# Kernel tuning notes

Hardware: AMD Instinct MI355X
Metric: run time of the kernel (lower is better)

## Reference

```python
import jax, jax.numpy as jnp
import numpy as np

NUM_HEADS = 8
HEAD_DIM = 64  # hidden_dim // num_heads = 512 // 8
THRESHOLD = 0.5


def setup_inputs() -> dict:
    key = jax.random.key(0)
    ks = jax.random.split(key, 12)
    B, T, D, Hd = 4, 1024, 512, 512
    s = 0.02
    inp = {
        'x': jax.random.normal(ks[0], (B, T, D), dtype=jnp.float32),
        'Wq': jax.random.normal(ks[1], (D, Hd), dtype=jnp.float32) * s,
        'bq': jnp.zeros((Hd,), jnp.float32),
        'Wk': jax.random.normal(ks[2], (D, Hd), dtype=jnp.float32) * s,
        'bk': jnp.zeros((Hd,), jnp.float32),
        'Wv': jax.random.normal(ks[3], (D, Hd), dtype=jnp.float32) * s,
        'bv': jnp.zeros((Hd,), jnp.float32),
        'conv_w': jax.random.normal(ks[4], (NUM_HEADS,), dtype=jnp.float32) * 0.3,
        'conv_b': jnp.zeros((1,), jnp.float32),
        'Wfh': jax.random.normal(ks[5], (Hd, Hd), dtype=jnp.float32) * s,
        'bfh': jnp.zeros((Hd,), jnp.float32),
        'Wfg': jax.random.normal(ks[6], (Hd, Hd), dtype=jnp.float32) * s,
        'bfg': jnp.zeros((Hd,), jnp.float32),
        'Wrh': jax.random.normal(ks[7], (Hd, Hd), dtype=jnp.float32) * s,
        'brh': jnp.zeros((Hd,), jnp.float32),
        'Wrg': jax.random.normal(ks[8], (Hd, Hd), dtype=jnp.float32) * s,
        'brg': jnp.zeros((Hd,), jnp.float32),
    }
    return inp


def reference(x, Wq, bq, Wk, bk, Wv, bv, conv_w, conv_b,
              Wfh, bfh, Wfg, bfg, Wrh, brh, Wrg, brg):
    B, T, D = x.shape
    H, hd = NUM_HEADS, HEAD_DIM
    scale = hd ** -0.5

    q = (x @ Wq + bq).reshape(B, T, H, hd).transpose(0, 2, 1, 3)  # [B,H,T,hd]
    k = (x @ Wk + bk).reshape(B, T, H, hd).transpose(0, 2, 1, 3)
    v = (x @ Wv + bv).reshape(B, T, H, hd).transpose(0, 2, 1, 3)

    scores = jnp.einsum('bhqd,bhkd->bhqk', q, k) * scale        # [B,H,T,T]
    A_t = jax.nn.softmax(scores, axis=-1)

    # cross-head 1x1 conv: weighted sum over heads -> [B,1,T,T]
    R_f = jax.nn.sigmoid(jnp.einsum('bhqk,h->bqk', A_t, conv_w) + conv_b[0])
    R_f = R_f[:, None]                                           # [B,1,T,T]
    M_f = (R_f <= THRESHOLD).astype(A_t.dtype)
    M_r = (1.0 - R_f <= THRESHOLD).astype(A_t.dtype)

    A_f = jax.nn.softmax(A_t * M_f, axis=-1)
    A_r = jax.nn.softmax(A_t * M_r, axis=-1)

    T_f = jnp.einsum('bhqk,bhkd->bhqd', A_f, v).transpose(0, 2, 1, 3).reshape(B, T, H * hd)
    T_r = jnp.einsum('bhqk,bhkd->bhqd', A_r, v).transpose(0, 2, 1, 3).reshape(B, T, H * hd)

    F_f = T_f @ Wfh + bfh
    G_f = jax.nn.sigmoid(T_f @ Wfg + bfg)
    F_r = T_r @ Wrh + brh
    G_r = jax.nn.sigmoid(T_r @ Wrg + brg)

    G_cat = jax.nn.softmax(jnp.stack([G_f, G_r], axis=-1), axis=-1)  # [B,T,Hd,2]
    F_t = F_f * G_cat[..., 0] + F_r * G_cat[..., 1]
    return F_t
```

## Files before the change

kernel.cpp:

```cpp
#include <hip/hip_runtime.h>
#include <hip/hip_bf16.h>
#include <stdint.h>

typedef short bf16x8 __attribute__((ext_vector_type(8)));
typedef float f32x4 __attribute__((ext_vector_type(4)));

__device__ __forceinline__ unsigned short f2bf(float f) {
  union { float f; unsigned int u; } v;
  v.f = f;
  unsigned int u = v.u;
  u = (u + 0x7fffu + ((u >> 16) & 1u)) >> 16;
  return (unsigned short)u;
}

__device__ __forceinline__ unsigned int cvt_pk_bf16(float lo, float hi) {
  unsigned int r;
  asm("v_cvt_pk_bf16_f32 %0, %1, %2" : "=v"(r) : "v"(lo), "v"(hi));
  return r;
}

typedef union { bf16x8 v; unsigned int u[4]; } frag_u;

__device__ __forceinline__ void gload16(const void* g, void* lds) {
  __builtin_amdgcn_global_load_lds(
      (const __attribute__((address_space(1))) unsigned int*)(unsigned long long)g,
      (__attribute__((address_space(3))) unsigned int*)(unsigned long long)(unsigned)(unsigned long long)lds,
      16, 0, 0);
}

__device__ __forceinline__ bf16x8 lds_frag(const unsigned short* t, int row, int ch4q) {
  return *(const bf16x8*)(t + row * 64 + ((ch4q ^ (row & 7)) << 3));
}


__global__ __launch_bounds__(256) void prep_kernel(
    const float* __restrict__ x,
    const float* __restrict__ Wq, const float* __restrict__ Wk, const float* __restrict__ Wv,
    const float* __restrict__ Wfh, const float* __restrict__ Wfg,
    const float* __restrict__ Wrh, const float* __restrict__ Wrg,
    unsigned short* __restrict__ xb, unsigned short* __restrict__ wt) {
  int bid = blockIdx.x;
  int tid = threadIdx.x;
  if (bid < 256) {
    const float4* xi = (const float4*)x;
#pragma unroll
    for (int rep = 0; rep < 8; rep++) {
      int i = bid * 256 + tid + rep * 65536;
      float4 v = xi[i];
      uint2 u;
      u.x = cvt_pk_bf16(v.x, v.y);
      u.y = cvt_pk_bf16(v.z, v.w);
      *(uint2*)&xb[(size_t)i * 4] = u;
    }
  } else {
    __shared__ float tile[64][65];
    int t = bid - 256;
    int mat = t >> 6;
    t &= 63;
    int tr = (t >> 3) * 64, tc = (t & 7) * 64;
    const float* W = (mat == 0) ? Wq : (mat == 1) ? Wk : (mat == 2) ? Wv
                   : (mat == 3) ? Wfh : (mat == 4) ? Wfg : (mat == 5) ? Wrh : Wrg;
    unsigned short* Wt = wt + (size_t)mat * 512 * 512;
    for (int rep = 0; rep < 16; rep++) {
      int idx = rep * 256 + tid;
      int r = idx >> 6, c = idx & 63;
      tile[r][c] = W[(tr + r) * 512 + tc + c];
    }
    __syncthreads();
    for (int rep = 0; rep < 16; rep++) {
      int idx = rep * 256 + tid;
      int r = idx >> 6, c = idx & 63;
      Wt[(tc + r) * 512 + tr + c] = f2bf(tile[c][r]);
    }
  }
}

__global__ __launch_bounds__(256, 2) void qkv_kernel(
    const unsigned short* __restrict__ xb,
    const unsigned short* __restrict__ wtq, const unsigned short* __restrict__ wtk,
    const unsigned short* __restrict__ wtv,
    const float* __restrict__ bq, const float* __restrict__ bk, const float* __restrict__ bv,
    unsigned short* __restrict__ Qfrag, unsigned short* __restrict__ Kfrag,
    unsigned short* __restrict__ Vfrag) {
  __shared__ __attribute__((aligned(16))) unsigned short smem[32768];
  unsigned short* st0 = smem;
  unsigned short* st1 = smem + 4608;
  unsigned short* st2 = smem + 9216;
  const int m0 = blockIdx.y * 64, n0 = blockIdx.x * 64;
  const int tid = threadIdx.x, w = tid >> 6, lane = tid & 63;
  const int c = lane & 15, quad = lane >> 4;
  const int wm = w & 1, wn = w >> 1;
  const int rsel = lane >> 3, csel = lane & 7;
  const int sc = csel ^ rsel;
  const char* Ag  = (const char*)xb  + (size_t)(m0 + w * 16 + rsel) * 1024 + sc * 16;
  const char* Bgq = (const char*)wtq + (size_t)(n0 + w * 16 + rsel) * 1024 + sc * 16;
  const char* Bgk = (const char*)wtk + (size_t)(n0 + w * 16 + rsel) * 1024 + sc * 16;
  const char* Bgv = (const char*)wtv + (size_t)(n0 + w * 16 + rsel) * 1024 + sc * 16;
  const int woff = w * 1024;

  f32x4 acc[3][2][2];
  f32x4 z4 = {0.f, 0.f, 0.f, 0.f};
#pragma unroll
  for (int o = 0; o < 3; o++)
#pragma unroll
    for (int i = 0; i < 2; i++)
#pragma unroll
      for (int j = 0; j < 2; j++) acc[o][i][j] = z4;

  {
    unsigned short* base = smem;
    gload16(Ag, base + woff);              gload16(Ag + 8192, base + woff + 512);
    gload16(Bgq, base + 4096 + woff);      gload16(Bgq + 8192, base + 4096 + woff + 512);
    gload16(Bgk, base + 8192 + woff);      gload16(Bgk + 8192, base + 8192 + woff + 512);
    gload16(Bgv, base + 12288 + woff);     gload16(Bgv + 8192, base + 12288 + woff + 512);
  }
  __syncthreads();

  for (int ks = 0; ks < 8; ks++) {
    unsigned short* cur = smem + (ks & 1) * 16384;
    if (ks < 7) {
      unsigned short* nxt = smem + ((ks + 1) & 1) * 16384;
      const int kb = (ks + 1) * 128;
      gload16(Ag + kb, nxt + woff);          gload16(Ag + kb + 8192, nxt + woff + 512);
      gload16(Bgq + kb, nxt + 4096 + woff);  gload16(Bgq + kb + 8192, nxt + 4096 + woff + 512);
      gload16(Bgk + kb, nxt + 8192 + woff);  gload16(Bgk + kb + 8192, nxt + 8192 + woff + 512);
      gload16(Bgv + kb, nxt + 12288 + woff); gload16(Bgv + kb + 8192, nxt + 12288 + woff + 512);
    }
#pragma unroll
    for (int ch = 0; ch < 2; ch++) {
      const int cq = ch * 4 + quad;
      bf16x8 a0 = lds_frag(cur, wm * 32 + c, cq);
      bf16x8 a1 = lds_frag(cur, wm * 32 + 16 + c, cq);
#pragma unroll
      for (int nt = 0; nt < 2; nt++) {
        const int rb = wn * 32 + nt * 16 + c;
        bf16x8 fq = lds_frag(cur + 4096, rb, cq);
        bf16x8 fk = lds_frag(cur + 8192, rb, cq);
        bf16x8 fv = lds_frag(cur + 12288, rb, cq);
        acc[0][0][nt] = __builtin_amdgcn_mfma_f32_16x16x32_bf16(a0, fq, acc[0][0][nt], 0, 0, 0);
        acc[0][1][nt] = __builtin_amdgcn_mfma_f32_16x16x32_bf16(a1, fq, acc[0][1][nt], 0, 0, 0);
        acc[1][0][nt] = __builtin_amdgcn_mfma_f32_16x16x32_bf16(a0, fk, acc[1][0][nt], 0, 0, 0);
        acc[1][1][nt] = __builtin_amdgcn_mfma_f32_16x16x32_bf16(a1, fk, acc[1][1][nt], 0, 0, 0);
        acc[2][0][nt] = __builtin_amdgcn_mfma_f32_16x16x32_bf16(a0, fv, acc[2][0][nt], 0, 0, 0);
        acc[2][1][nt] = __builtin_amdgcn_mfma_f32_16x16x32_bf16(a1, fv, acc[2][1][nt], 0, 0, 0);
      }
    }
    __syncthreads();
  }

#pragma unroll
  for (int ms = 0; ms < 2; ms++)
#pragma unroll
    for (int nt = 0; nt < 2; nt++) {
      int n_l = wn * 32 + nt * 16 + c;
      int n = n0 + n_l;
      float biasq = bq[n], biask = bk[n], biasv = bv[n];
#pragma unroll
      for (int r = 0; r < 4; r++) {
        int m_l = wm * 32 + ms * 16 + quad * 4 + r;
        st0[m_l * 72 + n_l] = f2bf((acc[0][ms][nt][r] + biasq) * 0.125f);
        st1[m_l * 72 + n_l] = f2bf(acc[1][ms][nt][r] + biask);
        st2[n_l * 72 + m_l] = f2bf(acc[2][ms][nt][r] + biasv);
      }
    }
  __syncthreads();

  {
    const int h = n0 >> 6;
    const int bb = m0 >> 10, t0b = (m0 & 1023) >> 4;
#pragma unroll
    for (int sub = 0; sub < 2; sub++) {
      uint4 vq = *(uint4*)&st0[(w * 16 + c) * 72 + sub * 32 + quad * 8];
      uint4 vk = *(uint4*)&st1[(w * 16 + c) * 72 + sub * 32 + quad * 8];
      size_t base = (size_t)((bb * 64 + t0b + w) * 8192) + h * 1024 + sub * 512 + lane * 8;
      *(uint4*)&Qfrag[base] = vq;
      *(uint4*)&Kfrag[base] = vk;
    }
    const int ktq = t0b + w;
    const int ktp = ktq >> 1, half = ktq & 1;
#pragma unroll
    for (int dm = 0; dm < 4; dm++) {
      uint2 vv = *(uint2*)&st2[(dm * 16 + c) * 72 + w * 16 + quad * 4];
      size_t base = (size_t)(bb * 8 + h) * 65536 + (size_t)(ktp * 4 + dm) * 512
                  + lane * 8 + half * 4;
      *(uint2*)&Vfrag[base] = vv;
    }
  }
}

__global__ __launch_bounds__(512, 2) void attn_kernel(
    const unsigned short* __restrict__ Qfrag, const unsigned short* __restrict__ Kfrag,
    const unsigned short* __restrict__ Vfrag,
    const float* __restrict__ conv_w, const float* __restrict__ conv_b,
    unsigned short* __restrict__ Tfb, unsigned short* __restrict__ Trb) {
  const int b = blockIdx.x, qt = blockIdx.y;
  const int tid = threadIdx.x, w = tid >> 6, lane = tid & 63;
  const int c = lane & 15, quad = lane >> 4;
  __shared__ float zbuf[8][16];
  __shared__ float izbuf[8][16];
  __shared__ __attribute__((aligned(16))) float red[2 * 8 * 4 * 64 * 4];
  __shared__ float zred[2][8][16];

  f32x4 z4 = {0.f, 0.f, 0.f, 0.f};
  const float cb = conv_b[0];
  const size_t qbase = (size_t)((b * 64 + qt) * 8192) + lane * 8;
  const size_t kb0 = (size_t)((b * 64 + w * 8) * 8192) + lane * 8;
  const size_t vb0 = (size_t)(b * 8) * 65536 + lane * 8;

  f32x4 g[8];
#pragma unroll
  for (int j = 0; j < 8; j++) g[j] = {cb, cb, cb, cb};

  for (int h = 0; h < 8; h++) {
    bf16x8 qf0 = *(const bf16x8*)&Qfrag[qbase + h * 1024];
    bf16x8 qf1 = *(const bf16x8*)&Qfrag[qbase + h * 1024 + 512];
    f32x4 p[8];
    float zh = 0.f;
#pragma unroll
    for (int j = 0; j < 8; j++) {
      const size_t kb = kb0 + (size_t)j * 8192 + h * 1024;
      bf16x8 kf0 = *(const bf16x8*)&Kfrag[kb];
      bf16x8 kf1 = *(const bf16x8*)&Kfrag[kb + 512];
      f32x4 s = __builtin_amdgcn_mfma_f32_16x16x32_bf16(kf0, qf0, z4, 0, 0, 0);
      s = __builtin_amdgcn_mfma_f32_16x16x32_bf16(kf1, qf1, s, 0, 0, 0);
      p[j][0] = __expf(s[0]); p[j][1] = __expf(s[1]);
      p[j][2] = __expf(s[2]); p[j][3] = __expf(s[3]);
      zh += (p[j][0] + p[j][1]) + (p[j][2] + p[j][3]);
    }
    zh += __shfl_xor(zh, 16); zh += __shfl_xor(zh, 32);
    __syncthreads();
    if (quad == 0) zbuf[w][c] = zh;
    __syncthreads();
    float Z = ((zbuf[0][c] + zbuf[1][c]) + (zbuf[2][c] + zbuf[3][c]))
            + ((zbuf[4][c] + zbuf[5][c]) + (zbuf[6][c] + zbuf[7][c]));
    const float izq = 1.0f / Z;
    if (w == 0 && quad == 0) izbuf[h][c] = izq;
    const float cwz = conv_w[h] * izq;
#pragma unroll
    for (int j = 0; j < 8; j++) {
      g[j][0] += cwz * p[j][0]; g[j][1] += cwz * p[j][1];
      g[j][2] += cwz * p[j][2]; g[j][3] += cwz * p[j][3];
    }
  }

  unsigned int mmx[4], mmy[4];
#pragma unroll
  for (int t = 0; t < 4; t++) {
    unsigned int p0 = 0, p1 = 0;
#pragma unroll
    for (int r = 0; r < 4; r++) {
      p0 |= ((g[2 * t][r] <= 0.f ? 1u : 0u) | (g[2 * t][r] >= 0.f ? 2u : 0u)) << (8 * r);
      p1 |= ((g[2 * t + 1][r] <= 0.f ? 1u : 0u) | (g[2 * t + 1][r] >= 0.f ? 2u : 0u)) << (8 * r);
    }
    mmx[t] = p0; mmy[t] = p1;
  }
  __syncthreads();

  frag_u ones;
  ones.u[0] = 0x3F803F80u; ones.u[1] = 0x3F803F80u;
  ones.u[2] = 0x3F803F80u; ones.u[3] = 0x3F803F80u;

  const int fr = w >> 2, dmslot = w & 3;
  const size_t tbase = (size_t)(b * 1024 + qt * 16 + c) * 512;
  unsigned short* dstsel = (fr == 0) ? Tfb : Trb;

  for (int h = 0; h < 8; h++) {
    bf16x8 qf0 = *(const bf16x8*)&Qfrag[qbase + h * 1024];
    bf16x8 qf1 = *(const bf16x8*)&Qfrag[qbase + h * 1024 + 512];
    const float iz_h = izbuf[h][c];
    f32x4 accf[4], accr[4];
#pragma unroll
    for (int i = 0; i < 4; i++) { accf[i] = z4; accr[i] = z4; }
    f32x4 zf4 = z4, zr4 = z4;
#pragma unroll
    for (int t = 0; t < 4; t++) {
      const size_t kba = kb0 + (size_t)(2 * t) * 8192 + h * 1024;
      const size_t kbb = kba + 8192;
      bf16x8 ka0 = *(const bf16x8*)&Kfrag[kba];
      bf16x8 ka1 = *(const bf16x8*)&Kfrag[kba + 512];
      bf16x8 kb0f = *(const bf16x8*)&Kfrag[kbb];
      bf16x8 kb1f = *(const bf16x8*)&Kfrag[kbb + 512];
      f32x4 sa = __builtin_amdgcn_mfma_f32_16x16x32_bf16(ka0, qf0, z4, 0, 0, 0);
      sa = __builtin_amdgcn_mfma_f32_16x16x32_bf16(ka1, qf1, sa, 0, 0, 0);
      f32x4 sb = __builtin_amdgcn_mfma_f32_16x16x32_bf16(kb0f, qf0, z4, 0, 0, 0);
      sb = __builtin_amdgcn_mfma_f32_16x16x32_bf16(kb1f, qf1, sb, 0, 0, 0);
      float ea[4], eb[4];
#pragma unroll
      for (int r = 0; r < 4; r++) {
        ea[r] = __expf(__expf(sa[r]) * iz_h);
        eb[r] = __expf(__expf(sb[r]) * iz_h);
      }
      frag_u pF, pR;
      pF.u[0] = cvt_pk_bf16((mmx[t] & 0x1u)       ? ea[0] : 1.f, (mmx[t] & 0x100u)     ? ea[1] : 1.f);
      pF.u[1] = cvt_pk_bf16((mmx[t] & 0x10000u)   ? ea[2] : 1.f, (mmx[t] & 0x1000000u) ? ea[3] : 1.f);
      pF.u[2] = cvt_pk_bf16((mmy[t] & 0x1u)       ? eb[0] : 1.f, (mmy[t] & 0x100u)     ? eb[1] : 1.f);
      pF.u[3] = cvt_pk_bf16((mmy[t] & 0x10000u)   ? eb[2] : 1.f, (mmy[t] & 0x1000000u) ? eb[3] : 1.f);
      pR.u[0] = cvt_pk_bf16((mmx[t] & 0x2u)       ? ea[0] : 1.f, (mmx[t] & 0x200u)     ? ea[1] : 1.f);
      pR.u[1] = cvt_pk_bf16((mmx[t] & 0x20000u)   ? ea[2] : 1.f, (mmx[t] & 0x2000000u) ? ea[3] : 1.f);
      pR.u[2] = cvt_pk_bf16((mmy[t] & 0x2u)       ? eb[0] : 1.f, (mmy[t] & 0x200u)     ? eb[1] : 1.f);
      pR.u[3] = cvt_pk_bf16((mmy[t] & 0x20000u)   ? eb[2] : 1.f, (mmy[t] & 0x2000000u) ? eb[3] : 1.f);
      zf4 = __builtin_amdgcn_mfma_f32_16x16x32_bf16(ones.v, pF.v, zf4, 0, 0, 0);
      zr4 = __builtin_amdgcn_mfma_f32_16x16x32_bf16(ones.v, pR.v, zr4, 0, 0, 0);
      const size_t vbh = vb0 + (size_t)h * 65536 + (size_t)((w * 4 + t) * 4) * 512;
#pragma unroll
      for (int dm = 0; dm < 4; dm++) {
        bf16x8 vf = *(const bf16x8*)&Vfrag[vbh + (size_t)dm * 512];
        accf[dm] = __builtin_amdgcn_mfma_f32_16x16x32_bf16(vf, pF.v, accf[dm], 0, 0, 0);
        accr[dm] = __builtin_amdgcn_mfma_f32_16x16x32_bf16(vf, pR.v, accr[dm], 0, 0, 0);
      }
    }
    __syncthreads();
#pragma unroll
    for (int dm = 0; dm < 4; dm++) {
      *(f32x4*)&red[(((0 * 8 + w) * 4 + dm) * 64 + lane) * 4] = accf[dm];
      *(f32x4*)&red[(((1 * 8 + w) * 4 + dm) * 64 + lane) * 4] = accr[dm];
    }
    if (quad == 0) { zred[0][w][c] = zf4[0]; zred[1][w][c] = zr4[0]; }
    __syncthreads();
    {
      f32x4 o = z4;
#pragma unroll
      for (int w2 = 0; w2 < 8; w2++)
        o += *(const f32x4*)&red[(((fr * 8 + w2) * 4 + dmslot) * 64 + lane) * 4];
      float Zq = 0.f;
#pragma unroll
      for (int w2 = 0; w2 < 8; w2++) Zq += zred[fr][w2][c];
      const float iz = 1.0f / Zq;
      uint2 u;
      u.x = cvt_pk_bf16(o[0] * iz, o[1] * iz);
      u.y = cvt_pk_bf16(o[2] * iz, o[3] * iz);
      *(uint2*)&dstsel[tbase + h * 64 + dmslot * 16 + quad * 4] = u;
    }
  }
}

__global__ __launch_bounds__(256, 2) void final_kernel(
    const unsigned short* __restrict__ Tfb, const unsigned short* __restrict__ Trb,
    const unsigned short* __restrict__ wfh, const unsigned short* __restrict__ wfg,
    const unsigned short* __restrict__ wrh, const unsigned short* __restrict__ wrg,
    const float* __restrict__ bfh, const float* __restrict__ bfg,
    const float* __restrict__ brh, const float* __restrict__ brg,
    float* __restrict__ out) {
  __shared__ __attribute__((aligned(16))) unsigned short smem[2][20480];
  const int m0 = blockIdx.y * 32, n0 = blockIdx.x * 64;
  const int tid = threadIdx.x, w = tid >> 6, lane = tid & 63;
  const int c = lane & 15, quad = lane >> 4;
  const int wm = w & 1, wn = w >> 1;
  const int rsel = lane >> 3, csel = lane & 7;
  const int sc = csel ^ rsel;
  const char* Agf = (const char*)Tfb + (size_t)(m0 + w * 8 + rsel) * 1024 + sc * 16;
  const char* Agr = (const char*)Trb + (size_t)(m0 + w * 8 + rsel) * 1024 + sc * 16;
  const char* Bg0 = (const char*)wfh + (size_t)(n0 + w * 16 + rsel) * 1024 + sc * 16;
  const char* Bg1 = (const char*)wfg + (size_t)(n0 + w * 16 + rsel) * 1024 + sc * 16;
  const char* Bg2 = (const char*)wrh + (size_t)(n0 + w * 16 + rsel) * 1024 + sc * 16;
  const char* Bg3 = (const char*)wrg + (size_t)(n0 + w * 16 + rsel) * 1024 + sc * 16;
  const int aoff = w * 512;
  const int boff = w * 1024;

  f32x4 acc[4][2];
  f32x4 z4 = {0.f, 0.f, 0.f, 0.f};
#pragma unroll
  for (int o = 0; o < 4; o++)
#pragma unroll
    for (int j = 0; j < 2; j++) acc[o][j] = z4;

  {
    unsigned short* nb = smem[0];
    gload16(Agf, nb + aoff);
    gload16(Agr, nb + 2048 + aoff);
    gload16(Bg0, nb + 4096 + boff);   gload16(Bg0 + 8192, nb + 4096 + boff + 512);
    gload16(Bg1, nb + 8192 + boff);   gload16(Bg1 + 8192, nb + 8192 + boff + 512);
    gload16(Bg2, nb + 12288 + boff);  gload16(Bg2 + 8192, nb + 12288 + boff + 512);
    gload16(Bg3, nb + 16384 + boff);  gload16(Bg3 + 8192, nb + 16384 + boff + 512);
  }
  __syncthreads();

  for (int ks = 0; ks < 8; ks++) {
    unsigned short* cur = smem[ks & 1];
    if (ks < 7) {
      unsigned short* nb = smem[(ks + 1) & 1];
      const int kb = (ks + 1) * 128;
      gload16(Agf + kb, nb + aoff);
      gload16(Agr + kb, nb + 2048 + aoff);
      gload16(Bg0 + kb, nb + 4096 + boff);   gload16(Bg0 + kb + 8192, nb + 4096 + boff + 512);
      gload16(Bg1 + kb, nb + 8192 + boff);   gload16(Bg1 + kb + 8192, nb + 8192 + boff + 512);
      gload16(Bg2 + kb, nb + 12288 + boff);  gload16(Bg2 + kb + 8192, nb + 12288 + boff + 512);
      gload16(Bg3 + kb, nb + 16384 + boff);  gload16(Bg3 + kb + 8192, nb + 16384 + boff + 512);
    }
#pragma unroll
    for (int ch = 0; ch < 2; ch++) {
      const int cq = ch * 4 + quad;
      bf16x8 af = lds_frag(cur, wm * 16 + c, cq);
      bf16x8 ar = lds_frag(cur + 2048, wm * 16 + c, cq);
#pragma unroll
      for (int nt = 0; nt < 2; nt++) {
        const int rb = wn * 32 + nt * 16 + c;
        bf16x8 f0 = lds_frag(cur + 4096, rb, cq);
        bf16x8 f1 = lds_frag(cur + 8192, rb, cq);
        bf16x8 f2 = lds_frag(cur + 12288, rb, cq);
        bf16x8 f3 = lds_frag(cur + 16384, rb, cq);
        acc[0][nt] = __builtin_amdgcn_mfma_f32_16x16x32_bf16(af, f0, acc[0][nt], 0, 0, 0);
        acc[1][nt] = __builtin_amdgcn_mfma_f32_16x16x32_bf16(af, f1, acc[1][nt], 0, 0, 0);
        acc[2][nt] = __builtin_amdgcn_mfma_f32_16x16x32_bf16(ar, f2, acc[2][nt], 0, 0, 0);
        acc[3][nt] = __builtin_amdgcn_mfma_f32_16x16x32_bf16(ar, f3, acc[3][nt], 0, 0, 0);
      }
    }
    __syncthreads();
  }

#pragma unroll
  for (int nt = 0; nt < 2; nt++) {
    int n = n0 + wn * 32 + nt * 16 + c;
    float b0 = bfh[n], b1 = bfg[n], b2 = brh[n], b3 = brg[n];
    int t0 = m0 + wm * 16 + quad * 4;
#pragma unroll
    for (int r = 0; r < 4; r++) {
      int t = t0 + r;
      float Ff = acc[0][nt][r] + b0;
      float Gf = 1.0f / (1.0f + __expf(-(acc[1][nt][r] + b1)));
      float Fr = acc[2][nt][r] + b2;
      float Gr = 1.0f / (1.0f + __expf(-(acc[3][nt][r] + b3)));
      float ef = __expf(Gf), er = __expf(Gr);
      out[(size_t)t * 512 + n] = (Ff * ef + Fr * er) / (ef + er);
    }
  }
}

extern "C" void kernel_launch(void* const* d_in, const int* in_sizes, int n_in,
                              void* d_out, int out_size, void* d_ws, size_t ws_size,
                              hipStream_t stream) {
  const float* x   = (const float*)d_in[0];
  const float* Wq  = (const float*)d_in[1];
  const float* bq  = (const float*)d_in[2];
  const float* Wk  = (const float*)d_in[3];
  const float* bk  = (const float*)d_in[4];
  const float* Wv  = (const float*)d_in[5];
  const float* bv  = (const float*)d_in[6];
  const float* cw  = (const float*)d_in[7];
  const float* cb  = (const float*)d_in[8];
  const float* Wfh = (const float*)d_in[9];
  const float* bfh = (const float*)d_in[10];
  const float* Wfg = (const float*)d_in[11];
  const float* bfg = (const float*)d_in[12];
  const float* Wrh = (const float*)d_in[13];
  const float* brh = (const float*)d_in[14];
  const float* Wrg = (const float*)d_in[15];
  const float* brg = (const float*)d_in[16];

  char* ws = (char*)d_ws;
  const size_t MB = 1024 * 1024;
  unsigned short* xb    = (unsigned short*)(ws + 0 * MB);
  unsigned short* Qfrag = (unsigned short*)(ws + 4 * MB);
  unsigned short* Kfrag = (unsigned short*)(ws + 8 * MB);
  unsigned short* Vfrag = (unsigned short*)(ws + 12 * MB);
  unsigned short* Tfb   = (unsigned short*)(ws + 16 * MB);
  unsigned short* Trb   = (unsigned short*)(ws + 20 * MB);
  unsigned short* wt    = (unsigned short*)(ws + 24 * MB);
  const size_t WSZ = 512 * 512;

  prep_kernel<<<704, 256, 0, stream>>>(x, Wq, Wk, Wv, Wfh, Wfg, Wrh, Wrg, xb, wt);
  qkv_kernel<<<dim3(8, 64), 256, 0, stream>>>(xb, wt + 0 * WSZ, wt + 1 * WSZ, wt + 2 * WSZ,
                                              bq, bk, bv, Qfrag, Kfrag, Vfrag);
  attn_kernel<<<dim3(4, 64), 512, 0, stream>>>(Qfrag, Kfrag, Vfrag, cw, cb, Tfb, Trb);
  final_kernel<<<dim3(8, 128), 256, 0, stream>>>(Tfb, Trb, wt + 3 * WSZ, wt + 4 * WSZ,
                                                 wt + 5 * WSZ, wt + 6 * WSZ,
                                                 bfh, bfg, brh, brg, (float*)d_out);
}
```

Before: 176.7 us.

## Fuse output gating GEMMs into attention kernel via LDS-staged T tiles

The attention kernel now writes its per-block T_f/T_r tiles (16 rows x 512) into shared memory instead of global buffers. Each of its 8 waves then computes a 64-column slice of the four output projections with MFMA and applies the gated softmax combine directly. This removes the separate final_kernel launch and the global round trip of the T buffers. In exchange, every attention block streams all four 512x512 weight matrices straight from global/L2 with no LDS reuse, and shared memory per block grows.

Result: slower. 224.5 us (+27.1%).

```diff
diff --git a/kernel.cpp b/kernel.cpp
--- a/kernel.cpp
+++ b/kernel.cpp
@@ -192,7 +192,11 @@
     const unsigned short* __restrict__ Qfrag, const unsigned short* __restrict__ Kfrag,
     const unsigned short* __restrict__ Vfrag,
     const float* __restrict__ conv_w, const float* __restrict__ conv_b,
-    unsigned short* __restrict__ Tfb, unsigned short* __restrict__ Trb) {
+    const unsigned short* __restrict__ wfh, const unsigned short* __restrict__ wfg,
+    const unsigned short* __restrict__ wrh, const unsigned short* __restrict__ wrg,
+    const float* __restrict__ bfh, const float* __restrict__ bfg,
+    const float* __restrict__ brh, const float* __restrict__ brg,
+    float* __restrict__ out) {
   const int b = blockIdx.x, qt = blockIdx.y;
   const int tid = threadIdx.x, w = tid >> 6, lane = tid & 63;
   const int c = lane & 15, quad = lane >> 4;
@@ -200,6 +204,7 @@
   __shared__ float izbuf[8][16];
   __shared__ __attribute__((aligned(16))) float red[2 * 8 * 4 * 64 * 4];
   __shared__ float zred[2][8][16];
+  __shared__ __attribute__((aligned(16))) unsigned short ts[2][16][520];
 
   f32x4 z4 = {0.f, 0.f, 0.f, 0.f};
   const float cb = conv_b[0];
@@ -261,8 +266,6 @@
   ones.u[2] = 0x3F803F80u; ones.u[3] = 0x3F803F80u;
 
   const int fr = w >> 2, dmslot = w & 3;
-  const size_t tbase = (size_t)(b * 1024 + qt * 16 + c) * 512;
-  unsigned short* dstsel = (fr == 0) ? Tfb : Trb;
 
   for (int h = 0; h < 8; h++) {
     bf16x8 qf0 = *(const bf16x8*)&Qfrag[qbase + h * 1024];
@@ -329,99 +332,52 @@
       uint2 u;
       u.x = cvt_pk_bf16(o[0] * iz, o[1] * iz);
       u.y = cvt_pk_bf16(o[2] * iz, o[3] * iz);
-      *(uint2*)&dstsel[tbase + h * 64 + dmslot * 16 + quad * 4] = u;
-    }
-  }
-}
-
-__global__ __launch_bounds__(256, 2) void final_kernel(
-    const unsigned short* __restrict__ Tfb, const unsigned short* __restrict__ Trb,
-    const unsigned short* __restrict__ wfh, const unsigned short* __restrict__ wfg,
-    const unsigned short* __restrict__ wrh, const unsigned short* __restrict__ wrg,
-    const float* __restrict__ bfh, const float* __restrict__ bfg,
-    const float* __restrict__ brh, const float* __restrict__ brg,
-    float* __restrict__ out) {
-  __shared__ __attribute__((aligned(16))) unsigned short smem[2][20480];
-  const int m0 = blockIdx.y * 32, n0 = blockIdx.x * 64;
-  const int tid = threadIdx.x, w = tid >> 6, lane = tid & 63;
-  const int c = lane & 15, quad = lane >> 4;
-  const int wm = w & 1, wn = w >> 1;
-  const int rsel = lane >> 3, csel = lane & 7;
-  const int sc = csel ^ rsel;
-  const char* Agf = (const char*)Tfb + (size_t)(m0 + w * 8 + rsel) * 1024 + sc * 16;
-  const char* Agr = (const char*)Trb + (size_t)(m0 + w * 8 + rsel) * 1024 + sc * 16;
-  const char* Bg0 = (const char*)wfh + (size_t)(n0 + w * 16 + rsel) * 1024 + sc * 16;
-  const char* Bg1 = (const char*)wfg + (size_t)(n0 + w * 16 + rsel) * 1024 + sc * 16;
-  const char* Bg2 = (const char*)wrh + (size_t)(n0 + w * 16 + rsel) * 1024 + sc * 16;
-  const char* Bg3 = (const char*)wrg + (size_t)(n0 + w * 16 + rsel) * 1024 + sc * 16;
-  const int aoff = w * 512;
-  const int boff = w * 1024;
-
-  f32x4 acc[4][2];
-  f32x4 z4 = {0.f, 0.f, 0.f, 0.f};
-#pragma unroll
-  for (int o = 0; o < 4; o++)
-#pragma unroll
-    for (int j = 0; j < 2; j++) acc[o][j] = z4;
+      *(uint2*)&ts[fr][c][h * 64 + dmslot * 16 + quad * 4] = u;
+    }
+  }
+  __syncthreads();
 
   {
-    unsigned short* nb = smem[0];
-    gload16(Agf, nb + aoff);
-    gload16(Agr, nb + 2048 + aoff);
-    gload16(Bg0, nb + 4096 + boff);   gload16(Bg0 + 8192, nb + 4096 + boff + 512);
-    gload16(Bg1, nb + 8192 + boff);   gload16(Bg1 + 8192, nb + 8192 + boff + 512);
-    gload16(Bg2, nb + 12288 + boff);  gload16(Bg2 + 8192, nb + 12288 + boff + 512);
-    gload16(Bg3, nb + 16384 + boff);  gload16(Bg3 + 8192, nb + 16384 + boff + 512);
-  }
-  __syncthreads();
-
-  for (int ks = 0; ks < 8; ks++) {
-    unsigned short* cur = smem[ks & 1];
-    if (ks < 7) {
-      unsigned short* nb = smem[(ks + 1) & 1];
-      const int kb = (ks + 1) * 128;
-      gload16(Agf + kb, nb + aoff);
-      gload16(Agr + kb, nb + 2048 + aoff);
-      gload16(Bg0 + kb, nb + 4096 + boff);   gload16(Bg0 + kb + 8192, nb + 4096 + boff + 512);
-      gload16(Bg1 + kb, nb + 8192 + boff);   gload16(Bg1 + kb + 8192, nb + 8192 + boff + 512);
-      gload16(Bg2 + kb, nb + 12288 + boff);  gload16(Bg2 + kb + 8192, nb + 12288 + boff + 512);
-      gload16(Bg3 + kb, nb + 16384 + boff);  gload16(Bg3 + kb + 8192, nb + 16384 + boff + 512);
-    }
-#pragma unroll
-    for (int ch = 0; ch < 2; ch++) {
-      const int cq = ch * 4 + quad;
-      bf16x8 af = lds_frag(cur, wm * 16 + c, cq);
-      bf16x8 ar = lds_frag(cur + 2048, wm * 16 + c, cq);
-#pragma unroll
-      for (int nt = 0; nt < 2; nt++) {
-        const int rb = wn * 32 + nt * 16 + c;
-        bf16x8 f0 = lds_frag(cur + 4096, rb, cq);
-        bf16x8 f1 = lds_frag(cur + 8192, rb, cq);
-        bf16x8 f2 = lds_frag(cur + 12288, rb, cq);
-        bf16x8 f3 = lds_frag(cur + 16384, rb, cq);
-        acc[0][nt] = __builtin_amdgcn_mfma_f32_16x16x32_bf16(af, f0, acc[0][nt], 0, 0, 0);
-        acc[1][nt] = __builtin_amdgcn_mfma_f32_16x16x32_bf16(af, f1, acc[1][nt], 0, 0, 0);
-        acc[2][nt] = __builtin_amdgcn_mfma_f32_16x16x32_bf16(ar, f2, acc[2][nt], 0, 0, 0);
-        acc[3][nt] = __builtin_amdgcn_mfma_f32_16x16x32_bf16(ar, f3, acc[3][nt], 0, 0, 0);
-      }
-    }
-    __syncthreads();
-  }
-
-#pragma unroll
-  for (int nt = 0; nt < 2; nt++) {
-    int n = n0 + wn * 32 + nt * 16 + c;
-    float b0 = bfh[n], b1 = bfg[n], b2 = brh[n], b3 = brg[n];
-    int t0 = m0 + wm * 16 + quad * 4;
-#pragma unroll
-    for (int r = 0; r < 4; r++) {
-      int t = t0 + r;
-      float Ff = acc[0][nt][r] + b0;
-      float Gf = 1.0f / (1.0f + __expf(-(acc[1][nt][r] + b1)));
-      float Fr = acc[2][nt][r] + b2;
-      float Gr = 1.0f / (1.0f + __expf(-(acc[3][nt][r] + b3)));
-      float ef = __expf(Gf), er = __expf(Gr);
-      out[(size_t)t * 512 + n] = (Ff * ef + Fr * er) / (ef + er);
+    const int n0w = w * 64;
+    const size_t r0 = (size_t)(b * 1024 + qt * 16);
+    f32x4 oa[4][4];
+#pragma unroll
+    for (int o = 0; o < 4; o++)
+#pragma unroll
+      for (int j = 0; j < 4; j++) oa[o][j] = z4;
+
+    for (int kk = 0; kk < 512; kk += 32) {
+      const int ko = kk + quad * 8;
+      bf16x8 aF = *(const bf16x8*)&ts[0][c][ko];
+      bf16x8 aR = *(const bf16x8*)&ts[1][c][ko];
+#pragma unroll
+      for (int nt = 0; nt < 4; nt++) {
+        const size_t bo = (size_t)(n0w + nt * 16 + c) * 512 + ko;
+        bf16x8 b0 = *(const bf16x8*)&wfh[bo];
+        bf16x8 b1 = *(const bf16x8*)&wfg[bo];
+        bf16x8 b2 = *(const bf16x8*)&wrh[bo];
+        bf16x8 b3 = *(const bf16x8*)&wrg[bo];
+        oa[0][nt] = __builtin_amdgcn_mfma_f32_16x16x32_bf16(aF, b0, oa[0][nt], 0, 0, 0);
+        oa[1][nt] = __builtin_amdgcn_mfma_f32_16x16x32_bf16(aF, b1, oa[1][nt], 0, 0, 0);
+        oa[2][nt] = __builtin_amdgcn_mfma_f32_16x16x32_bf16(aR, b2, oa[2][nt], 0, 0, 0);
+        oa[3][nt] = __builtin_amdgcn_mfma_f32_16x16x32_bf16(aR, b3, oa[3][nt], 0, 0, 0);
+      }
+    }
+
+#pragma unroll
+    for (int nt = 0; nt < 4; nt++) {
+      int n = n0w + nt * 16 + c;
+      float b0 = bfh[n], b1 = bfg[n], b2 = brh[n], b3 = brg[n];
+#pragma unroll
+      for (int r = 0; r < 4; r++) {
+        size_t t = r0 + quad * 4 + r;
+        float Ff = oa[0][nt][r] + b0;
+        float Gf = 1.0f / (1.0f + __expf(-(oa[1][nt][r] + b1)));
+        float Fr = oa[2][nt][r] + b2;
+        float Gr = 1.0f / (1.0f + __expf(-(oa[3][nt][r] + b3)));
+        float ef = __expf(Gf), er = __expf(Gr);
+        out[t * 512 + n] = (Ff * ef + Fr * er) / (ef + er);
+      }
     }
   }
 }
@@ -453,16 +409,14 @@
   unsigned short* Qfrag = (unsigned short*)(ws + 4 * MB);
   unsigned short* Kfrag = (unsigned short*)(ws + 8 * MB);
   unsigned short* Vfrag = (unsigned short*)(ws + 12 * MB);
-  unsigned short* Tfb   = (unsigned short*)(ws + 16 * MB);
-  unsigned short* Trb   = (unsigned short*)(ws + 20 * MB);
   unsigned short* wt    = (unsigned short*)(ws + 24 * MB);
   const size_t WSZ = 512 * 512;
 
   prep_kernel<<<704, 256, 0, stream>>>(x, Wq, Wk, Wv, Wfh, Wfg, Wrh, Wrg, xb, wt);
   qkv_kernel<<<dim3(8, 64), 256, 0, stream>>>(xb, wt + 0 * WSZ, wt + 1 * WSZ, wt + 2 * WSZ,
                                               bq, bk, bv, Qfrag, Kfrag, Vfrag);
-  attn_kernel<<<dim3(4, 64), 512, 0, stream>>>(Qfrag, Kfrag, Vfrag, cw, cb, Tfb, Trb);
-  final_kernel<<<dim3(8, 128), 256, 0, stream>>>(Tfb, Trb, wt + 3 * WSZ, wt + 4 * WSZ,
-                                                 wt + 5 * WSZ, wt + 6 * WSZ,
-                                                 bfh, bfg, brh, brg, (float*)d_out);
-}
+  attn_kernel<<<dim3(4, 64), 512, 0, stream>>>(Qfrag, Kfrag, Vfrag, cw, cb,
+                                               wt + 3 * WSZ, wt + 4 * WSZ,
+                                               wt + 5 * WSZ, wt + 6 * WSZ,
+                                               bfh, bfg, brh, brg, (float*)d_out);
+}
```
